# Kernel tuning notes

Measured on AMD Instinct MI355X. Metric: run time of the kernel, lower is better.

Reference implementation:

```python
import jax, jax.numpy as jnp
import numpy as np

IN_C = 512
OUT_C = 1024
N = 8192


def _xavier(key, shape):
    fan_in, fan_out = shape[1], shape[0]
    limit = float(np.sqrt(6.0 / (fan_in + fan_out)))
    return jax.random.uniform(key, shape, jnp.float32, -limit, limit)


def setup_inputs() -> dict:
    key = jax.random.key(0)
    ks = jax.random.split(key, 20)
    inp = {
        'x': jax.random.normal(ks[0], (IN_C, N), jnp.float32),
        'c_prev_dim0': jax.random.normal(ks[1], (OUT_C, N), jnp.float32),
        'h_prev_dim0': jax.random.normal(ks[2], (OUT_C, N), jnp.float32),
        'c_prev_dim1': jax.random.normal(ks[3], (OUT_C, N), jnp.float32),
        'h_prev_dim1': jax.random.normal(ks[4], (OUT_C, N), jnp.float32),
    }
    names_x = ['w_ii', 'w_if', 'w_ig', 'w_io']
    names_h = ['w_hi', 'w_hf', 'w_hg', 'w_ho']
    names_b = ['b_i', 'b_f', 'b_g', 'b_o']
    k = 5
    for n in names_x:
        inp[n] = _xavier(ks[k], (OUT_C, IN_C)); k += 1
    for n in names_h:
        inp[n] = _xavier(ks[k], (OUT_C, OUT_C)); k += 1
    for n in names_b:
        inp[n] = _xavier(ks[k], (OUT_C, 1)); k += 1
    inp['weighted_sum'] = jax.random.uniform(ks[k], (2,), jnp.float32)
    return inp


def reference(x, c_prev_dim0, h_prev_dim0, c_prev_dim1, h_prev_dim1,
              w_ii, w_if, w_ig, w_io,
              w_hi, w_hf, w_hg, w_ho,
              b_i, b_f, b_g, b_o,
              weighted_sum):
    # Input projections shared by both spatial directions: (out, N)
    xi = w_ii @ x
    xf = w_if @ x
    xg = w_ig @ x
    xo = w_io @ x

    def gates(h_prev, c_prev):
        i = jax.nn.sigmoid(xi + w_hi @ h_prev + b_i)
        f = jax.nn.sigmoid(xf + w_hf @ h_prev + b_f)
        g = jnp.tanh(xg + w_hg @ h_prev + b_g)
        o = jax.nn.sigmoid(xo + w_ho @ h_prev + b_o)
        c = f * c_prev + i * g
        h = o * jnp.tanh(c)
        return c, h

    ct0, ht0 = gates(h_prev_dim0, c_prev_dim0)
    ct1, ht1 = gates(h_prev_dim1, c_prev_dim1)
    ct = ct0 * weighted_sum[0] + ct1 * weighted_sum[1]
    ht = ht0 * weighted_sum[0] + ht1 * weighted_sum[1]
    return ct, ht
```

## Files before the change

### kernel.cpp

```cpp
#include <hip/hip_runtime.h>
#include <cstdint>
#include <cstddef>

#define IN_C  512
#define OUT_C 1024
#define NSAMP 8192
#define KTOT  1536

typedef __bf16 bf16x8 __attribute__((ext_vector_type(8)));
typedef float  f32x4  __attribute__((ext_vector_type(4)));

#define SBAR()   __builtin_amdgcn_s_barrier()
#define SFENCE() __builtin_amdgcn_sched_barrier(0)
#define VM0()    asm volatile("s_waitcnt vmcnt(0)")

__device__ __forceinline__ unsigned short f2bf(float f) {
    unsigned int u = __float_as_uint(f);
    u += 0x7FFFu + ((u >> 16) & 1u);
    return (unsigned short)(u >> 16);
}
__device__ __forceinline__ float sigmoid_f(float x) { return 1.0f / (1.0f + __expf(-x)); }
__device__ __forceinline__ float tanh_f(float x) {
    float e = __expf(2.0f * x);
    return 1.0f - 2.0f / (e + 1.0f);
}

__global__ void tcvt_kernel(const float* __restrict__ in, unsigned short* __restrict__ out,
                            int R, int C) {
    __shared__ float t[32][33];
    const int tx = threadIdx.x, ty = threadIdx.y;
    const int c0 = blockIdx.x * 32, r0 = blockIdx.y * 32;
#pragma unroll
    for (int i = 0; i < 4; ++i)
        t[ty + i * 8][tx] = in[(size_t)(r0 + ty + i * 8) * C + (c0 + tx)];
    __syncthreads();
#pragma unroll
    for (int i = 0; i < 4; ++i)
        out[(size_t)(c0 + ty + i * 8) * R + (r0 + tx)] = f2bf(t[tx][ty + i * 8]);
}

__global__ void packA_kernel(const float* __restrict__ x0, const float* __restrict__ x1,
                             const float* __restrict__ x2, const float* __restrict__ x3,
                             const float* __restrict__ h0, const float* __restrict__ h1,
                             const float* __restrict__ h2, const float* __restrict__ h3,
                             unsigned short* __restrict__ Ap) {
    const int idx = blockIdx.x * 256 + threadIdx.x;
    const int m = idx / 192, k8 = idx % 192;
    const int g = m & 3, r = m >> 2;
    const float* src;
    if (k8 < 64) {
        const float* a = (g & 2) ? ((g & 1) ? x3 : x2) : ((g & 1) ? x1 : x0);
        src = a + (size_t)r * IN_C + k8 * 8;
    } else {
        const float* a = (g & 2) ? ((g & 1) ? h3 : h2) : ((g & 1) ? h1 : h0);
        src = a + (size_t)r * OUT_C + (k8 - 64) * 8;
    }
    float4 v0 = reinterpret_cast<const float4*>(src)[0];
    float4 v1 = reinterpret_cast<const float4*>(src)[1];
    ushort4 o0, o1;
    o0.x = f2bf(v0.x); o0.y = f2bf(v0.y); o0.z = f2bf(v0.z); o0.w = f2bf(v0.w);
    o1.x = f2bf(v1.x); o1.y = f2bf(v1.y); o1.z = f2bf(v1.z); o1.w = f2bf(v1.w);
    ushort4* dst = reinterpret_cast<ushort4*>(Ap + (size_t)m * KTOT + k8 * 8);
    dst[0] = o0; dst[1] = o1;
}

__global__ __launch_bounds__(512, 2) void mdlstm_main(
    const unsigned short* __restrict__ Ap,
    const unsigned short* __restrict__ xT,
    const unsigned short* __restrict__ h0T,
    const unsigned short* __restrict__ h1T,
    const float* __restrict__ b_i, const float* __restrict__ b_f,
    const float* __restrict__ b_g, const float* __restrict__ b_o,
    const float* __restrict__ cp0, const float* __restrict__ cp1,
    const float* __restrict__ wsum,
    float* __restrict__ out)
{
    __shared__ __align__(16) unsigned char smem[131072];

    const int tid  = threadIdx.x;
    const int lane = tid & 63;
    const int wid  = tid >> 6;
    const int wm   = wid >> 2;
    const int wn   = wid & 3;
    const int g4   = lane >> 4;
    const int l16  = lane & 15;

    const int by    = blockIdx.y;
    const int bcol  = blockIdx.x * 128;
    const int browM = by * 256;

    f32x4 acc[8][4];
#pragma unroll
    for (int mf = 0; mf < 8; ++mf)
#pragma unroll
        for (int nf = 0; nf < 4; ++nf)
            acc[mf][nf] = (f32x4){0.f, 0.f, 0.f, 0.f};

    auto stage_A = [&](int P, int hA, int j1) {
#pragma unroll
        for (int c = 0; c < 2; ++c) {
            const int u    = c * 8192 + tid * 16;
            const int rloc = (u >> 6) & 127;
            const int kb   = (u & 63) ^ (((u >> 7) & 3) << 4);
            const char* src = (const char*)Ap
                + ((size_t)(browM + hA * 128 + rloc) * KTOT + j1 * 64 + c * 32) * 2 + kb;
            __builtin_amdgcn_global_load_lds((const unsigned int*)src,
                (unsigned int*)(smem + P * 65536 + hA * 16384 + u), 16, 0, 0);
        }
    };
    auto stage_B = [&](int P, int d, int j2) {
#pragma unroll
        for (int c = 0; c < 2; ++c) {
            const int u    = c * 8192 + tid * 16;
            const int rloc = (u >> 6) & 127;
            const int kb   = (u & 63) ^ (((u >> 7) & 3) << 4);
            const char* src;
            if (j2 < 8) {
                src = (const char*)xT + ((size_t)(bcol + rloc) * IN_C + j2 * 64 + c * 32) * 2 + kb;
            } else {
                const unsigned short* hsrc = d ? h1T : h0T;
                src = (const char*)hsrc + ((size_t)(bcol + rloc) * OUT_C + (j2 - 8) * 64 + c * 32) * 2 + kb;
            }
            __builtin_amdgcn_global_load_lds((const unsigned int*)src,
                (unsigned int*)(smem + P * 65536 + 32768 + d * 16384 + u), 16, 0, 0);
        }
    };

    auto swzb = [](int u) { return u ^ (((u >> 7) & 3) << 4); };
    auto fragA = [&](int P, int mf, int kk) -> bf16x8 {
        const int u = kk * 8192 + (mf * 16 + l16) * 64 + g4 * 16;
        return *reinterpret_cast<const bf16x8*>(smem + P * 65536 + wm * 16384 + swzb(u));
    };
    auto fragB = [&](int P, int nf, int kk) -> bf16x8 {
        const int u = kk * 8192 + ((wn & 1) * 64 + nf * 16 + l16) * 64 + g4 * 16;
        return *reinterpret_cast<const bf16x8*>(smem + P * 65536 + 32768 + (wn >> 1) * 16384 + swzb(u));
    };

    bf16x8 aFa[2][2], aFb[2][2];
    bf16x8 bF[4][2];

    auto cluster = [&](bf16x8 (&aF)[2][2], int M) {
        __builtin_amdgcn_s_setprio(1);
#pragma unroll
        for (int kk = 0; kk < 2; ++kk)
#pragma unroll
            for (int mi = 0; mi < 2; ++mi)
#pragma unroll
                for (int nf = 0; nf < 4; ++nf)
                    acc[M + mi][nf] = __builtin_amdgcn_mfma_f32_16x16x32_bf16(
                        aF[mi][kk], bF[nf][kk], acc[M + mi][nf], 0, 0, 0);
        __builtin_amdgcn_s_setprio(0);
    };
    auto loadA = [&](bf16x8 (&aF)[2][2], int P, int mf) {
#pragma unroll
        for (int kk = 0; kk < 2; ++kk) { aF[0][kk] = fragA(P, mf, kk); aF[1][kk] = fragA(P, mf + 1, kk); }
    };
    auto loadB = [&](int P) {
#pragma unroll
        for (int nf = 0; nf < 4; ++nf)
#pragma unroll
            for (int kk = 0; kk < 2; ++kk) bF[nf][kk] = fragB(P, nf, kk);
    };

    auto ktile = [&](int j, int P, int PN) {
        const bool st = (j < 23);
        loadB(P);
        loadA(aFa, P, 0);
        loadA(aFb, P, 2);
        cluster(aFa, 0);
        loadA(aFa, P, 4);
        if (st) { stage_A(PN, 0, j + 1); stage_A(PN, 1, j + 1); }
        cluster(aFb, 2);
        loadA(aFb, P, 6);
        if (st) { stage_B(PN, 0, j + 1); stage_B(PN, 1, j + 1); }
        cluster(aFa, 4);
        cluster(aFb, 6);
        SFENCE(); VM0(); SFENCE();
        SBAR();
    };

    stage_A(0, 0, 0); stage_A(0, 1, 0);
    stage_B(0, 0, 0); stage_B(0, 1, 0);
    SFENCE(); VM0(); SFENCE();
    SBAR();

#pragma unroll 1
    for (int jj = 0; jj < 12; ++jj) {
        ktile(2 * jj,     0, 1);
        ktile(2 * jj + 1, 1, 0);
    }

    const float w0 = wsum[0], w1 = wsum[1];
    const int   d  = wn >> 1;
    const float* cp = d ? cp1 : cp0;
    const float wd  = d ? w1 : w0;

    float rc[8][4], rh[8][4];
#pragma unroll
    for (int mf = 0; mf < 8; ++mf) {
        const int orow = by * 64 + wm * 32 + mf * 4 + g4;
        const float bi = b_i[orow], bff = b_f[orow], bg = b_g[orow], bo = b_o[orow];
#pragma unroll
        for (int nf = 0; nf < 4; ++nf) {
            const int scol = bcol + (wn & 1) * 64 + nf * 16 + l16;
            float i_ = sigmoid_f(acc[mf][nf][0] + bi);
            float f_ = sigmoid_f(acc[mf][nf][1] + bff);
            float g_ = tanh_f  (acc[mf][nf][2] + bg);
            float o_ = sigmoid_f(acc[mf][nf][3] + bo);
            float cc = f_ * cp[(size_t)orow * NSAMP + scol] + i_ * g_;
            float hh = o_ * tanh_f(cc);
            rc[mf][nf] = wd * cc;
            rh[mf][nf] = wd * hh;
        }
    }

    float* ex = (float*)smem;
    const int rbase = (wm * 2 + (wn & 1)) * 4096;
    if (d == 1) {
#pragma unroll
        for (int mf = 0; mf < 8; ++mf)
#pragma unroll
            for (int nf = 0; nf < 4; ++nf) {
                const int slot = rbase + (mf * 4 + nf) * 64 + lane;
                ex[slot]        = rc[mf][nf];
                ex[slot + 2048] = rh[mf][nf];
            }
    }
    SBAR();
    if (d == 0) {
#pragma unroll
        for (int mf = 0; mf < 8; ++mf) {
            const int orow = by * 64 + wm * 32 + mf * 4 + g4;
#pragma unroll
            for (int nf = 0; nf < 4; ++nf) {
                const int scol = bcol + (wn & 1) * 64 + nf * 16 + l16;
                const int slot = rbase + (mf * 4 + nf) * 64 + lane;
                out[(size_t)orow * NSAMP + scol] = rc[mf][nf] + ex[slot];
                out[(size_t)OUT_C * NSAMP + (size_t)orow * NSAMP + scol] = rh[mf][nf] + ex[slot + 2048];
            }
        }
    }
}

extern "C" void kernel_launch(void* const* d_in, const int* in_sizes, int n_in,
                              void* d_out, int out_size, void* d_ws, size_t ws_size,
                              hipStream_t stream) {
    (void)in_sizes; (void)n_in; (void)out_size; (void)ws_size;

    const float* x    = (const float*)d_in[0];
    const float* cp0  = (const float*)d_in[1];
    const float* hp0  = (const float*)d_in[2];
    const float* cp1  = (const float*)d_in[3];
    const float* hp1  = (const float*)d_in[4];
    const float* b_i  = (const float*)d_in[13];
    const float* b_f  = (const float*)d_in[14];
    const float* b_g  = (const float*)d_in[15];
    const float* b_o  = (const float*)d_in[16];
    const float* wsum = (const float*)d_in[17];
    float* out = (float*)d_out;

    char* ws = (char*)d_ws;
    unsigned short* xT  = (unsigned short*)(ws);
    unsigned short* h0T = (unsigned short*)(ws + (size_t)8  * 1024 * 1024);
    unsigned short* h1T = (unsigned short*)(ws + (size_t)24 * 1024 * 1024);
    unsigned short* Ap  = (unsigned short*)(ws + (size_t)40 * 1024 * 1024);

    dim3 tb(32, 8);
    tcvt_kernel<<<dim3(NSAMP / 32, IN_C  / 32), tb, 0, stream>>>(x,   xT,  IN_C,  NSAMP);
    tcvt_kernel<<<dim3(NSAMP / 32, OUT_C / 32), tb, 0, stream>>>(hp0, h0T, OUT_C, NSAMP);
    tcvt_kernel<<<dim3(NSAMP / 32, OUT_C / 32), tb, 0, stream>>>(hp1, h1T, OUT_C, NSAMP);

    packA_kernel<<<(4096 * 192) / 256, 256, 0, stream>>>(
        (const float*)d_in[5], (const float*)d_in[6], (const float*)d_in[7], (const float*)d_in[8],
        (const float*)d_in[9], (const float*)d_in[10], (const float*)d_in[11], (const float*)d_in[12],
        Ap);

    mdlstm_main<<<dim3(NSAMP / 128, OUT_C / 64), 512, 0, stream>>>(
        Ap, xT, h0T, h1T, b_i, b_f, b_g, b_o, cp0, cp1, wsum, out);
}
```

Before: 271.2 us.

## Load A-operand fragments straight from global into registers, bypassing LDS

The weight (A) tile is no longer staged through shared memory. Each wave now reads its own A fragments from global memory directly into registers, with the next tile's first half prefetched at the end of each k-tile, and uses a partial vmcnt wait so those loads can stay in flight across the barrier. LDS shrinks to 64 KB, holding only the double-buffered B tile with an adjusted read swizzle, which may let two blocks fit per CU. In exchange, the four waves that share a row group each fetch the same A rows, so A traffic through L2 rises, and the mid-tile A loads expose global latency right before the MFMAs that consume them.

```diff
diff --git a/kernel.cpp b/kernel.cpp
--- a/kernel.cpp
+++ b/kernel.cpp
@@ -12,6 +12,7 @@
 
 #define SBAR()   __builtin_amdgcn_s_barrier()
 #define SFENCE() __builtin_amdgcn_sched_barrier(0)
+#define VM8()    asm volatile("s_waitcnt vmcnt(8)")
 #define VM0()    asm volatile("s_waitcnt vmcnt(0)")
 
 __device__ __forceinline__ unsigned short f2bf(float f) {
@@ -75,7 +76,7 @@
     const float* __restrict__ wsum,
     float* __restrict__ out)
 {
-    __shared__ __align__(16) unsigned char smem[131072];
+    __shared__ __align__(16) unsigned char smem[65536];
 
     const int tid  = threadIdx.x;
     const int lane = tid & 63;
@@ -96,18 +97,6 @@
         for (int nf = 0; nf < 4; ++nf)
             acc[mf][nf] = (f32x4){0.f, 0.f, 0.f, 0.f};
 
-    auto stage_A = [&](int P, int hA, int j1) {
-#pragma unroll
-        for (int c = 0; c < 2; ++c) {
-            const int u    = c * 8192 + tid * 16;
-            const int rloc = (u >> 6) & 127;
-            const int kb   = (u & 63) ^ (((u >> 7) & 3) << 4);
-            const char* src = (const char*)Ap
-                + ((size_t)(browM + hA * 128 + rloc) * KTOT + j1 * 64 + c * 32) * 2 + kb;
-            __builtin_amdgcn_global_load_lds((const unsigned int*)src,
-                (unsigned int*)(smem + P * 65536 + hA * 16384 + u), 16, 0, 0);
-        }
-    };
     auto stage_B = [&](int P, int d, int j2) {
 #pragma unroll
         for (int c = 0; c < 2; ++c) {
@@ -122,24 +111,31 @@
                 src = (const char*)hsrc + ((size_t)(bcol + rloc) * OUT_C + (j2 - 8) * 64 + c * 32) * 2 + kb;
             }
             __builtin_amdgcn_global_load_lds((const unsigned int*)src,
-                (unsigned int*)(smem + P * 65536 + 32768 + d * 16384 + u), 16, 0, 0);
-        }
-    };
-
-    auto swzb = [](int u) { return u ^ (((u >> 7) & 3) << 4); };
-    auto fragA = [&](int P, int mf, int kk) -> bf16x8 {
-        const int u = kk * 8192 + (mf * 16 + l16) * 64 + g4 * 16;
-        return *reinterpret_cast<const bf16x8*>(smem + P * 65536 + wm * 16384 + swzb(u));
-    };
+                (unsigned int*)(smem + P * 32768 + d * 16384 + u), 16, 0, 0);
+        }
+    };
+
     auto fragB = [&](int P, int nf, int kk) -> bf16x8 {
-        const int u = kk * 8192 + ((wn & 1) * 64 + nf * 16 + l16) * 64 + g4 * 16;
-        return *reinterpret_cast<const bf16x8*>(smem + P * 65536 + 32768 + (wn >> 1) * 16384 + swzb(u));
-    };
-
-    bf16x8 aFa[2][2], aFb[2][2];
+        const int row = (wn & 1) * 64 + nf * 16 + l16;
+        const int u = kk * 8192 + row * 64 + ((g4 * 16) ^ (((row >> 1) & 3) << 4));
+        return *reinterpret_cast<const bf16x8*>(smem + P * 32768 + (wn >> 1) * 16384 + u);
+    };
+
+    bf16x8 aA[4][2];
     bf16x8 bF[4][2];
 
-    auto cluster = [&](bf16x8 (&aF)[2][2], int M) {
+    auto loadAglobal = [&](int j, int mfbase) {
+#pragma unroll
+        for (int q = 0; q < 4; ++q)
+#pragma unroll
+            for (int kk = 0; kk < 2; ++kk) {
+                const int row = browM + wm * 128 + (mfbase + q) * 16 + l16;
+                aA[q][kk] = *reinterpret_cast<const bf16x8*>(
+                    Ap + (size_t)row * KTOT + j * 64 + kk * 32 + g4 * 8);
+            }
+    };
+
+    auto cluster = [&](int M, int i0) {
         __builtin_amdgcn_s_setprio(1);
 #pragma unroll
         for (int kk = 0; kk < 2; ++kk)
@@ -148,13 +144,9 @@
 #pragma unroll
                 for (int nf = 0; nf < 4; ++nf)
                     acc[M + mi][nf] = __builtin_amdgcn_mfma_f32_16x16x32_bf16(
-                        aF[mi][kk], bF[nf][kk], acc[M + mi][nf], 0, 0, 0);
+                        aA[i0 + mi][kk], bF[nf][kk], acc[M + mi][nf], 0, 0, 0);
         __builtin_amdgcn_s_setprio(0);
     };
-    auto loadA = [&](bf16x8 (&aF)[2][2], int P, int mf) {
-#pragma unroll
-        for (int kk = 0; kk < 2; ++kk) { aF[0][kk] = fragA(P, mf, kk); aF[1][kk] = fragA(P, mf + 1, kk); }
-    };
     auto loadB = [&](int P) {
 #pragma unroll
         for (int nf = 0; nf < 4; ++nf)
@@ -162,32 +154,34 @@
             for (int kk = 0; kk < 2; ++kk) bF[nf][kk] = fragB(P, nf, kk);
     };
 
-    auto ktile = [&](int j, int P, int PN) {
-        const bool st = (j < 23);
+    auto ktile = [&](int j, int P, int PN, bool last) {
+        SFENCE();
         loadB(P);
-        loadA(aFa, P, 0);
-        loadA(aFb, P, 2);
-        cluster(aFa, 0);
-        loadA(aFa, P, 4);
-        if (st) { stage_A(PN, 0, j + 1); stage_A(PN, 1, j + 1); }
-        cluster(aFb, 2);
-        loadA(aFb, P, 6);
-        if (st) { stage_B(PN, 0, j + 1); stage_B(PN, 1, j + 1); }
-        cluster(aFa, 4);
-        cluster(aFb, 6);
-        SFENCE(); VM0(); SFENCE();
+        cluster(0, 0);
+        if (!last) stage_B(PN, 0, j + 1);
+        cluster(2, 2);
+        loadAglobal(j, 4);
+        if (!last) stage_B(PN, 1, j + 1);
+        cluster(4, 0);
+        cluster(6, 2);
+        if (!last) {
+            loadAglobal(j + 1, 0);
+            SFENCE(); VM8(); SFENCE();
+        } else {
+            SFENCE(); VM0(); SFENCE();
+        }
         SBAR();
     };
 
-    stage_A(0, 0, 0); stage_A(0, 1, 0);
     stage_B(0, 0, 0); stage_B(0, 1, 0);
-    SFENCE(); VM0(); SFENCE();
+    loadAglobal(0, 0);
+    SFENCE(); VM8(); SFENCE();
     SBAR();
 
 #pragma unroll 1
     for (int jj = 0; jj < 12; ++jj) {
-        ktile(2 * jj,     0, 1);
-        ktile(2 * jj + 1, 1, 0);
+        ktile(2 * jj,     0, 1, false);
+        ktile(2 * jj + 1, 1, 0, 2 * jj + 1 == 23);
     }
 
     const float w0 = wsum[0], w1 = wsum[1];
```

Result: slower. 455.7 us (+68.0%).

## Shrink GEMM block tile to 128x64 with 4 waves and 64KB LDS

Applied to the files above, without the earlier changes.

Halves the main kernel's block tile (128 A-rows x 64 columns per direction) and uses 256 threads per block with 64KB of shared memory instead of 512 threads and 128KB. Each wave now owns one direction and a 64-row slice, and the grid grows fourfold. The shared-memory swizzle changes to a row-based XOR applied at load time. The aim is more resident blocks per CU and better latency hiding, at the cost of less operand reuse per block, more global and L2 traffic, and a shorter MFMA run per k-tile to cover the staging loads.

```diff
diff --git a/kernel.cpp b/kernel.cpp
--- a/kernel.cpp
+++ b/kernel.cpp
@@ -64,7 +64,7 @@
     dst[0] = o0; dst[1] = o1;
 }
 
-__global__ __launch_bounds__(512, 2) void mdlstm_main(
+__global__ __launch_bounds__(256, 2) void mdlstm_main(
     const unsigned short* __restrict__ Ap,
     const unsigned short* __restrict__ xT,
     const unsigned short* __restrict__ h0T,
@@ -75,65 +75,70 @@
     const float* __restrict__ wsum,
     float* __restrict__ out)
 {
-    __shared__ __align__(16) unsigned char smem[131072];
+    __shared__ __align__(16) unsigned char smem[65536];
 
     const int tid  = threadIdx.x;
     const int lane = tid & 63;
     const int wid  = tid >> 6;
-    const int wm   = wid >> 2;
-    const int wn   = wid & 3;
+    const int dir  = wid & 1;
+    const int wm   = wid >> 1;
     const int g4   = lane >> 4;
     const int l16  = lane & 15;
 
     const int by    = blockIdx.y;
-    const int bcol  = blockIdx.x * 128;
-    const int browM = by * 256;
-
-    f32x4 acc[8][4];
-#pragma unroll
-    for (int mf = 0; mf < 8; ++mf)
+    const int bcol  = blockIdx.x * 64;
+    const int browM = by * 128;
+
+    f32x4 acc[4][4];
+#pragma unroll
+    for (int mf = 0; mf < 4; ++mf)
 #pragma unroll
         for (int nf = 0; nf < 4; ++nf)
             acc[mf][nf] = (f32x4){0.f, 0.f, 0.f, 0.f};
 
-    auto stage_A = [&](int P, int hA, int j1) {
+    auto stage_A = [&](int P, int j1) {
+#pragma unroll
+        for (int c = 0; c < 4; ++c) {
+            const int u    = c * 4096 + tid * 16;
+            const int kk   = u >> 13;
+            const int rloc = (u >> 6) & 127;
+            const int kb   = u & 63;
+            const char* src = (const char*)Ap
+                + ((size_t)(browM + rloc) * KTOT + j1 * 64 + kk * 32) * 2
+                + (kb ^ (((rloc >> 1) & 3) << 4));
+            __builtin_amdgcn_global_load_lds((const unsigned int*)src,
+                (unsigned int*)(smem + P * 32768 + u), 16, 0, 0);
+        }
+    };
+    auto stage_B = [&](int P, int d, int j2) {
 #pragma unroll
         for (int c = 0; c < 2; ++c) {
-            const int u    = c * 8192 + tid * 16;
-            const int rloc = (u >> 6) & 127;
-            const int kb   = (u & 63) ^ (((u >> 7) & 3) << 4);
-            const char* src = (const char*)Ap
-                + ((size_t)(browM + hA * 128 + rloc) * KTOT + j1 * 64 + c * 32) * 2 + kb;
-            __builtin_amdgcn_global_load_lds((const unsigned int*)src,
-                (unsigned int*)(smem + P * 65536 + hA * 16384 + u), 16, 0, 0);
-        }
-    };
-    auto stage_B = [&](int P, int d, int j2) {
-#pragma unroll
-        for (int c = 0; c < 2; ++c) {
-            const int u    = c * 8192 + tid * 16;
-            const int rloc = (u >> 6) & 127;
-            const int kb   = (u & 63) ^ (((u >> 7) & 3) << 4);
+            const int u    = c * 4096 + tid * 16;
+            const int rloc = (u >> 6) & 63;
+            const int kb   = u & 63;
             const char* src;
             if (j2 < 8) {
-                src = (const char*)xT + ((size_t)(bcol + rloc) * IN_C + j2 * 64 + c * 32) * 2 + kb;
+                src = (const char*)xT + ((size_t)(bcol + rloc) * IN_C + j2 * 64 + c * 32) * 2
+                      + (kb ^ (((rloc >> 1) & 3) << 4));
             } else {
                 const unsigned short* hsrc = d ? h1T : h0T;
-                src = (const char*)hsrc + ((size_t)(bcol + rloc) * OUT_C + (j2 - 8) * 64 + c * 32) * 2 + kb;
+                src = (const char*)hsrc + ((size_t)(bcol + rloc) * OUT_C + (j2 - 8) * 64 + c * 32) * 2
+                      + (kb ^ (((rloc >> 1) & 3) << 4));
             }
             __builtin_amdgcn_global_load_lds((const unsigned int*)src,
-                (unsigned int*)(smem + P * 65536 + 32768 + d * 16384 + u), 16, 0, 0);
-        }
-    };
-
-    auto swzb = [](int u) { return u ^ (((u >> 7) & 3) << 4); };
+                (unsigned int*)(smem + P * 32768 + 16384 + d * 8192 + u), 16, 0, 0);
+        }
+    };
+
     auto fragA = [&](int P, int mf, int kk) -> bf16x8 {
-        const int u = kk * 8192 + (mf * 16 + l16) * 64 + g4 * 16;
-        return *reinterpret_cast<const bf16x8*>(smem + P * 65536 + wm * 16384 + swzb(u));
+        const int row = wm * 64 + mf * 16 + l16;
+        const int u = kk * 8192 + row * 64 + ((g4 * 16) ^ (((row >> 1) & 3) << 4));
+        return *reinterpret_cast<const bf16x8*>(smem + P * 32768 + u);
     };
     auto fragB = [&](int P, int nf, int kk) -> bf16x8 {
-        const int u = kk * 8192 + ((wn & 1) * 64 + nf * 16 + l16) * 64 + g4 * 16;
-        return *reinterpret_cast<const bf16x8*>(smem + P * 65536 + 32768 + (wn >> 1) * 16384 + swzb(u));
+        const int row = nf * 16 + l16;
+        const int u = kk * 4096 + row * 64 + ((g4 * 16) ^ (((row >> 1) & 3) << 4));
+        return *reinterpret_cast<const bf16x8*>(smem + P * 32768 + 16384 + dir * 8192 + u);
     };
 
     bf16x8 aFa[2][2], aFb[2][2];
@@ -166,20 +171,15 @@
         const bool st = (j < 23);
         loadB(P);
         loadA(aFa, P, 0);
+        cluster(aFa, 0);
         loadA(aFb, P, 2);
-        cluster(aFa, 0);
-        loadA(aFa, P, 4);
-        if (st) { stage_A(PN, 0, j + 1); stage_A(PN, 1, j + 1); }
+        if (st) { stage_A(PN, j + 1); stage_B(PN, 0, j + 1); stage_B(PN, 1, j + 1); }
         cluster(aFb, 2);
-        loadA(aFb, P, 6);
-        if (st) { stage_B(PN, 0, j + 1); stage_B(PN, 1, j + 1); }
-        cluster(aFa, 4);
-        cluster(aFb, 6);
         SFENCE(); VM0(); SFENCE();
         SBAR();
     };
 
-    stage_A(0, 0, 0); stage_A(0, 1, 0);
+    stage_A(0, 0);
     stage_B(0, 0, 0); stage_B(0, 1, 0);
     SFENCE(); VM0(); SFENCE();
     SBAR();
@@ -190,19 +190,17 @@
         ktile(2 * jj + 1, 1, 0);
     }
 
-    const float w0 = wsum[0], w1 = wsum[1];
-    const int   d  = wn >> 1;
-    const float* cp = d ? cp1 : cp0;
-    const float wd  = d ? w1 : w0;
-
-    float rc[8][4], rh[8][4];
-#pragma unroll
-    for (int mf = 0; mf < 8; ++mf) {
-        const int orow = by * 64 + wm * 32 + mf * 4 + g4;
+    const float wd  = wsum[dir];
+    const float* cp = dir ? cp1 : cp0;
+
+    float rc[4][4], rh[4][4];
+#pragma unroll
+    for (int mf = 0; mf < 4; ++mf) {
+        const int orow = by * 32 + wm * 16 + mf * 4 + g4;
         const float bi = b_i[orow], bff = b_f[orow], bg = b_g[orow], bo = b_o[orow];
 #pragma unroll
         for (int nf = 0; nf < 4; ++nf) {
-            const int scol = bcol + (wn & 1) * 64 + nf * 16 + l16;
+            const int scol = bcol + nf * 16 + l16;
             float i_ = sigmoid_f(acc[mf][nf][0] + bi);
             float f_ = sigmoid_f(acc[mf][nf][1] + bff);
             float g_ = tanh_f  (acc[mf][nf][2] + bg);
@@ -215,26 +213,25 @@
     }
 
     float* ex = (float*)smem;
-    const int rbase = (wm * 2 + (wn & 1)) * 4096;
-    if (d == 1) {
-#pragma unroll
-        for (int mf = 0; mf < 8; ++mf)
+    if (dir == 1) {
+#pragma unroll
+        for (int mf = 0; mf < 4; ++mf)
 #pragma unroll
             for (int nf = 0; nf < 4; ++nf) {
-                const int slot = rbase + (mf * 4 + nf) * 64 + lane;
+                const int slot = wm * 1024 + (mf * 4 + nf) * 64 + lane;
                 ex[slot]        = rc[mf][nf];
                 ex[slot + 2048] = rh[mf][nf];
             }
     }
     SBAR();
-    if (d == 0) {
-#pragma unroll
-        for (int mf = 0; mf < 8; ++mf) {
-            const int orow = by * 64 + wm * 32 + mf * 4 + g4;
+    if (dir == 0) {
+#pragma unroll
+        for (int mf = 0; mf < 4; ++mf) {
+            const int orow = by * 32 + wm * 16 + mf * 4 + g4;
 #pragma unroll
             for (int nf = 0; nf < 4; ++nf) {
-                const int scol = bcol + (wn & 1) * 64 + nf * 16 + l16;
-                const int slot = rbase + (mf * 4 + nf) * 64 + lane;
+                const int scol = bcol + nf * 16 + l16;
+                const int slot = wm * 1024 + (mf * 4 + nf) * 64 + lane;
                 out[(size_t)orow * NSAMP + scol] = rc[mf][nf] + ex[slot];
                 out[(size_t)OUT_C * NSAMP + (size_t)orow * NSAMP + scol] = rh[mf][nf] + ex[slot + 2048];
             }
@@ -275,6 +272,6 @@
         (const float*)d_in[9], (const float*)d_in[10], (const float*)d_in[11], (const float*)d_in[12],
         Ap);
 
-    mdlstm_main<<<dim3(NSAMP / 128, OUT_C / 64), 512, 0, stream>>>(
+    mdlstm_main<<<dim3(NSAMP / 64, OUT_C / 32), 256, 0, stream>>>(
         Ap, xT, h0T, h1T, b_i, b_f, b_g, b_o, cp0, cp1, wsum, out);
 }
```

Measured after the change: 278.8 us. 2.8% more time.
